# Kernel optimization log

Hardware: AMD Instinct MI355X
Metric: run time of the kernel (lower is better)

## Reference

```python
import jax, jax.numpy as jnp
import numpy as np

BN_EPS = 1e-5
LEAKY_SLOPE = 0.01

N_TOTAL, FEAT_DIM = 100000, 128
N_BATCH, K = 50000, 16
EMBED_DIM = 128


def setup_inputs() -> dict:
    key = jax.random.key(0)
    k1, k2, k3 = jax.random.split(key, 3)
    raw_features = jax.random.normal(k1, (N_TOTAL, FEAT_DIM), dtype=jnp.float32)
    weight = jax.random.normal(k2, (FEAT_DIM, EMBED_DIM), dtype=jnp.float32) * (1.0 / np.sqrt(FEAT_DIM))
    gamma = jnp.ones((EMBED_DIM,), dtype=jnp.float32)
    beta = jnp.zeros((EMBED_DIM,), dtype=jnp.float32)
    neigh_idx = jax.random.randint(k3, (N_BATCH, K), 0, N_TOTAL, dtype=jnp.int64)
    return {"raw_features": raw_features, "weight": weight, "gamma": gamma,
            "beta": beta, "neigh_idx": neigh_idx}


def reference(raw_features, weight, gamma, beta, neigh_idx):
    # Mean aggregation over sampled neighbors: [N_BATCH, K, F] -> [N_BATCH, F]
    neigh_feats = jnp.mean(raw_features[neigh_idx], axis=1)
    # Dense transform: [N_BATCH, EMBED_DIM]
    x = neigh_feats @ weight
    # BatchNorm1d (training mode: batch statistics, biased variance)
    mean = jnp.mean(x, axis=0)
    var = jnp.var(x, axis=0)
    x = (x - mean) * jax.lax.rsqrt(var + BN_EPS) * gamma + beta
    # LeakyReLU (default negative_slope=0.01)
    return jnp.where(x >= 0, x, LEAKY_SLOPE * x)
```

## Files before the change

### kernel.cpp

```cpp
#include <hip/hip_runtime.h>
#include <hip/hip_bf16.h>
#include <hip/hip_fp16.h>


#define NTOTAL 100000
#define FEAT   128
#define NB     50000
#define KNEI   16
#define NTILES (NB / 16)

#define OFF_STATS 0
#define OFF_WT    1024
#define OFF_RAWH  33792
#define OFF_NF    (33792 + 25600000)
#define WS_NEEDED (OFF_NF + 12800000)

typedef float f32x4 __attribute__((ext_vector_type(4)));
typedef short bf16x8 __attribute__((ext_vector_type(8)));
typedef _Float16 f16x8 __attribute__((ext_vector_type(8)));

__device__ __forceinline__ unsigned short f2bf(float f) {
    union { float f; unsigned u; } v; v.f = f;
    unsigned r = v.u + 0x7FFF + ((v.u >> 16) & 1);
    return (unsigned short)(r >> 16);
}

__device__ __forceinline__ unsigned h2add(unsigned a, unsigned b) {
    union { unsigned u; __half2 h; } x, y, r;
    x.u = a; y.u = b; r.h = __hadd2(x.h, y.h);
    return r.u;
}
__device__ __forceinline__ unsigned h2scale16(unsigned a) {
    union { unsigned u; __half2 h; } x, c, r;
    x.u = a; c.u = 0x2C002C00u;
    r.h = __hmul2(x.h, c.h);
    return r.u;
}

__global__ __launch_bounds__(256) void enc_conv(
    const float* __restrict__ raw, const float* __restrict__ W,
    unsigned short* __restrict__ rawh, unsigned short* __restrict__ Wt,
    float* __restrict__ gstats)
{
    const int t = threadIdx.x;
    if (blockIdx.x < 64) {
        int e = blockIdx.x * 256 + t;
        int n = e >> 7, k = e & 127;
        union { unsigned short s; __half h; } c; c.h = __float2half(W[k * FEAT + n]);
        Wt[e] = c.s;
    }
    if (blockIdx.x == 64 && t < 2 * FEAT) gstats[t] = 0.f;

    const float4* raw4 = (const float4*)raw;
    uint2* rh = (uint2*)rawh;
    const int NQ = NTOTAL * FEAT / 4;
    for (int e = blockIdx.x * 256 + t; e < NQ; e += gridDim.x * 256) {
        float4 v = raw4[e];
        union { unsigned u; __half2 h; } lo, hi;
        lo.h = __float22half2_rn(make_float2(v.x, v.y));
        hi.h = __float22half2_rn(make_float2(v.z, v.w));
        uint2 o; o.x = lo.u; o.y = hi.u;
        rh[e] = o;
    }
}

__global__ __launch_bounds__(256, 5) void enc_gather(
    const unsigned short* __restrict__ rawh, const int* __restrict__ idx,
    unsigned short* __restrict__ nf)
{
    const int t = threadIdx.x;
    const int lane = t & 63;
    const int w = (blockIdx.x * 256 + t) >> 6;
    const int r0 = w * 4;
    const int s = lane >> 4, c = lane & 15;

    const int iv = idx[r0 * KNEI + lane];

    uint4 v[16];
    #pragma unroll
    for (int k = 0; k < KNEI; ++k) {
        int ik = __shfl(iv, s * 16 + k);
        v[k] = *(const uint4*)&rawh[(size_t)ik * FEAT + c * 8];
    }
    #pragma unroll
    for (int st = 8; st >= 1; st >>= 1) {
        #pragma unroll
        for (int k = 0; k < 8; ++k) {
            if (k < st) {
                v[k].x = h2add(v[k].x, v[k + st].x);
                v[k].y = h2add(v[k].y, v[k + st].y);
                v[k].z = h2add(v[k].z, v[k + st].z);
                v[k].w = h2add(v[k].w, v[k + st].w);
            }
        }
    }
    uint4 o;
    o.x = h2scale16(v[0].x); o.y = h2scale16(v[0].y);
    o.z = h2scale16(v[0].z); o.w = h2scale16(v[0].w);
    *(uint4*)&nf[(size_t)(r0 + s) * FEAT + c * 8] = o;
}

__global__ __launch_bounds__(256, 4) void enc_mm(
    const unsigned short* __restrict__ nf, const unsigned short* __restrict__ Wt,
    float* __restrict__ out, float* __restrict__ gstats)
{
    const int t = threadIdx.x;
    const int lane = t & 63;
    const int wv = t >> 6;
    const int ln = lane & 15, qd = lane >> 4;
    const int n0 = wv * 32 + ln, n1 = n0 + 16;

    f16x8 b0[4], b1[4];
    #pragma unroll
    for (int kt = 0; kt < 4; ++kt) {
        const int k0 = kt * 32 + qd * 8;
        b0[kt] = *(const f16x8*)&Wt[n0 * FEAT + k0];
        b1[kt] = *(const f16x8*)&Wt[n1 * FEAT + k0];
    }

    float s1a = 0.f, s2a = 0.f, s1b = 0.f, s2b = 0.f;

    for (int tile = blockIdx.x; tile < NTILES; tile += gridDim.x) {
        const int i0 = tile * 16;
        f32x4 acc0 = {0.f, 0.f, 0.f, 0.f}, acc1 = {0.f, 0.f, 0.f, 0.f};
        #pragma unroll
        for (int kt = 0; kt < 4; ++kt) {
            const int k0 = kt * 32 + qd * 8;
            f16x8 a = *(const f16x8*)&nf[(size_t)(i0 + ln) * FEAT + k0];
            acc0 = __builtin_amdgcn_mfma_f32_16x16x32_f16(a, b0[kt], acc0, 0, 0, 0);
            acc1 = __builtin_amdgcn_mfma_f32_16x16x32_f16(a, b1[kt], acc1, 0, 0, 0);
        }
        #pragma unroll
        for (int ri = 0; ri < 4; ++ri) {
            const int row = i0 + qd * 4 + ri;
            float v0 = acc0[ri], v1 = acc1[ri];
            out[row * FEAT + n0] = v0;
            out[row * FEAT + n1] = v1;
            s1a += v0; s2a += v0 * v0;
            s1b += v1; s2b += v1 * v1;
        }
    }

    s1a += __shfl_down(s1a, 32); s1a += __shfl_down(s1a, 16);
    s2a += __shfl_down(s2a, 32); s2a += __shfl_down(s2a, 16);
    s1b += __shfl_down(s1b, 32); s1b += __shfl_down(s1b, 16);
    s2b += __shfl_down(s2b, 32); s2b += __shfl_down(s2b, 16);
    if (qd == 0) {
        atomicAdd(&gstats[n0], s1a);
        atomicAdd(&gstats[FEAT + n0], s2a);
        atomicAdd(&gstats[n1], s1b);
        atomicAdd(&gstats[FEAT + n1], s2b);
    }
}

__global__ __launch_bounds__(256) void enc_bn(
    float* __restrict__ out, const float* __restrict__ gstats,
    const float* __restrict__ gamma, const float* __restrict__ beta)
{
    __shared__ float sScale[FEAT], sShift[FEAT];
    const int t = threadIdx.x;
    if (t < FEAT) {
        float s1 = gstats[t], s2 = gstats[FEAT + t];
        float mean = s1 * (1.0f / NB);
        float var = s2 * (1.0f / NB) - mean * mean;
        float sc = gamma[t] * rsqrtf(var + 1e-5f);
        sScale[t] = sc;
        sShift[t] = beta[t] - mean * sc;
    }
    __syncthreads();
    const int f4 = (t & 31) * 4;
    const float4 sc = *(const float4*)&sScale[f4];
    const float4 sh = *(const float4*)&sShift[f4];
    const int total4 = NB * FEAT / 4;
    float4* o4 = (float4*)out;
    for (int e = blockIdx.x * 256 + t; e < total4; e += gridDim.x * 256) {
        float4 v = o4[e];
        float4 r; float y;
        y = v.x * sc.x + sh.x; r.x = (y >= 0.f) ? y : 0.01f * y;
        y = v.y * sc.y + sh.y; r.y = (y >= 0.f) ? y : 0.01f * y;
        y = v.z * sc.z + sh.z; r.z = (y >= 0.f) ? y : 0.01f * y;
        y = v.w * sc.w + sh.w; r.w = (y >= 0.f) ? y : 0.01f * y;
        o4[e] = r;
    }
}

#define WT_LD 136
#define A_LD  136
__global__ __launch_bounds__(256, 4) void enc_gemm_f(
    const float* __restrict__ raw, const float* __restrict__ W,
    const int* __restrict__ idx, float* __restrict__ out,
    float* __restrict__ gstats)
{
    __shared__ unsigned short sWt[128 * WT_LD];
    __shared__ unsigned short sA[16 * A_LD];
    __shared__ int sidx[256];
    const int t = threadIdx.x;
    #pragma unroll 4
    for (int i = 0; i < 64; ++i) {
        int e = t + i * 256;
        int f = e >> 7, n = e & 127;
        sWt[n * WT_LD + f] = f2bf(W[e]);
    }
    const int lane = t & 63, wv = t >> 6, ln = lane & 15, qd = lane >> 4;
    const int c = t & 31, g = t >> 5;
    const int n0 = wv * 32 + ln, n1 = n0 + 16;
    float s1a = 0.f, s2a = 0.f, s1b = 0.f, s2b = 0.f;
    const float4* raw4 = (const float4*)raw;
    for (int tile = blockIdx.x; tile < NTILES; tile += gridDim.x) {
        const int i0 = tile * 16;
        __syncthreads();
        sidx[t] = idx[i0 * KNEI + t];
        __syncthreads();
        #pragma unroll
        for (int rr = 0; rr < 2; ++rr) {
            const int r = g * 2 + rr;
            const int* ip = &sidx[r * KNEI];
            float4 acc = {0.f, 0.f, 0.f, 0.f};
            #pragma unroll
            for (int k = 0; k < KNEI; ++k) {
                float4 v = raw4[(size_t)ip[k] * 32 + c];
                acc.x += v.x; acc.y += v.y; acc.z += v.z; acc.w += v.w;
            }
            ushort4 b;
            b.x = f2bf(acc.x * 0.0625f); b.y = f2bf(acc.y * 0.0625f);
            b.z = f2bf(acc.z * 0.0625f); b.w = f2bf(acc.w * 0.0625f);
            *(ushort4*)&sA[r * A_LD + c * 4] = b;
        }
        __syncthreads();
        f32x4 acc0 = {0.f, 0.f, 0.f, 0.f}, acc1 = {0.f, 0.f, 0.f, 0.f};
        #pragma unroll
        for (int kt = 0; kt < 4; ++kt) {
            const int k0 = kt * 32 + qd * 8;
            bf16x8 a  = *(const bf16x8*)&sA[ln * A_LD + k0];
            bf16x8 bb0 = *(const bf16x8*)&sWt[n0 * WT_LD + k0];
            bf16x8 bb1 = *(const bf16x8*)&sWt[n1 * WT_LD + k0];
            acc0 = __builtin_amdgcn_mfma_f32_16x16x32_bf16(a, bb0, acc0, 0, 0, 0);
            acc1 = __builtin_amdgcn_mfma_f32_16x16x32_bf16(a, bb1, acc1, 0, 0, 0);
        }
        #pragma unroll
        for (int ri = 0; ri < 4; ++ri) {
            const int row = i0 + qd * 4 + ri;
            float v0 = acc0[ri], v1 = acc1[ri];
            out[row * FEAT + n0] = v0;
            out[row * FEAT + n1] = v1;
            s1a += v0; s2a += v0 * v0;
            s1b += v1; s2b += v1 * v1;
        }
    }
    s1a += __shfl_down(s1a, 32); s1a += __shfl_down(s1a, 16);
    s2a += __shfl_down(s2a, 32); s2a += __shfl_down(s2a, 16);
    s1b += __shfl_down(s1b, 32); s1b += __shfl_down(s1b, 16);
    s2b += __shfl_down(s2b, 32); s2b += __shfl_down(s2b, 16);
    if (qd == 0) {
        atomicAdd(&gstats[n0], s1a);
        atomicAdd(&gstats[FEAT + n0], s2a);
        atomicAdd(&gstats[n1], s1b);
        atomicAdd(&gstats[FEAT + n1], s2b);
    }
}

extern "C" void kernel_launch(void* const* d_in, const int* in_sizes, int n_in,
                              void* d_out, int out_size, void* d_ws, size_t ws_size,
                              hipStream_t stream) {
    const float* raw   = (const float*)d_in[0];
    const float* W     = (const float*)d_in[1];
    const float* gamma = (const float*)d_in[2];
    const float* beta  = (const float*)d_in[3];
    const int*   idx   = (const int*)d_in[4];
    float* out = (float*)d_out;

    char* ws = (char*)d_ws;
    float* gstats = (float*)(ws + OFF_STATS);

    if (ws_size >= WS_NEEDED) {
        unsigned short* Wt   = (unsigned short*)(ws + OFF_WT);
        unsigned short* rawh = (unsigned short*)(ws + OFF_RAWH);
        unsigned short* nf   = (unsigned short*)(ws + OFF_NF);
        enc_conv<<<2048, 256, 0, stream>>>(raw, W, rawh, Wt, gstats);
        enc_gather<<<3125, 256, 0, stream>>>(rawh, idx, nf);
        enc_mm<<<782, 256, 0, stream>>>(nf, Wt, out, gstats);
        enc_bn<<<1024, 256, 0, stream>>>(out, gstats, gamma, beta);
    } else {
        hipMemsetAsync(gstats, 0, 2 * FEAT * sizeof(float), stream);
        enc_gemm_f<<<1024, 256, 0, stream>>>(raw, W, idx, out, gstats);
        enc_bn<<<1024, 256, 0, stream>>>(out, gstats, gamma, beta);
    }
}
```

Baseline: 163.9 us.

## Fuse neighbor gather and GEMM into one kernel with per-wave tiles

Merges the gather/mean kernel and the MFMA matmul kernel into one. Each wave gathers a 16-row tile of fp16 features into shared memory and immediately multiplies it against W held in shared memory, so the intermediate neighbor-feature buffer never goes through global memory. BN statistics are first reduced in shared memory, then flushed with one atomic per column per block, which cuts global atomics. The trade-off is lower occupancy (launch bounds 3, larger LDS use) and a serial gather-then-MFMA step inside each wave that can expose gather latency.

```diff
diff --git a/kernel.cpp b/kernel.cpp
--- a/kernel.cpp
+++ b/kernel.cpp
@@ -12,19 +12,19 @@
 #define OFF_STATS 0
 #define OFF_WT    1024
 #define OFF_RAWH  33792
-#define OFF_NF    (33792 + 25600000)
-#define WS_NEEDED (OFF_NF + 12800000)
+#define WS_NEEDED (OFF_RAWH + 25600000)
 
 typedef float f32x4 __attribute__((ext_vector_type(4)));
 typedef short bf16x8 __attribute__((ext_vector_type(8)));
 typedef _Float16 f16x8 __attribute__((ext_vector_type(8)));
+
+#define ALD 136
 
 __device__ __forceinline__ unsigned short f2bf(float f) {
     union { float f; unsigned u; } v; v.f = f;
     unsigned r = v.u + 0x7FFF + ((v.u >> 16) & 1);
     return (unsigned short)(r >> 16);
 }
-
 __device__ __forceinline__ unsigned h2add(unsigned a, unsigned b) {
     union { unsigned u; __half2 h; } x, y, r;
     x.u = a; y.u = b; r.h = __hadd2(x.h, y.h);
@@ -64,93 +64,116 @@
     }
 }
 
-__global__ __launch_bounds__(256, 5) void enc_gather(
-    const unsigned short* __restrict__ rawh, const int* __restrict__ idx,
-    unsigned short* __restrict__ nf)
+__global__ __launch_bounds__(256, 3) void enc_fused(
+    const unsigned short* __restrict__ rawh, const unsigned short* __restrict__ Wt,
+    const int* __restrict__ idx, float* __restrict__ out,
+    float* __restrict__ gstats)
 {
-    const int t = threadIdx.x;
-    const int lane = t & 63;
-    const int w = (blockIdx.x * 256 + t) >> 6;
-    const int r0 = w * 4;
-    const int s = lane >> 4, c = lane & 15;
-
-    const int iv = idx[r0 * KNEI + lane];
-
-    uint4 v[16];
-    #pragma unroll
-    for (int k = 0; k < KNEI; ++k) {
-        int ik = __shfl(iv, s * 16 + k);
-        v[k] = *(const uint4*)&rawh[(size_t)ik * FEAT + c * 8];
-    }
-    #pragma unroll
-    for (int st = 8; st >= 1; st >>= 1) {
-        #pragma unroll
-        for (int k = 0; k < 8; ++k) {
-            if (k < st) {
-                v[k].x = h2add(v[k].x, v[k + st].x);
-                v[k].y = h2add(v[k].y, v[k + st].y);
-                v[k].z = h2add(v[k].z, v[k + st].z);
-                v[k].w = h2add(v[k].w, v[k + st].w);
-            }
-        }
-    }
-    uint4 o;
-    o.x = h2scale16(v[0].x); o.y = h2scale16(v[0].y);
-    o.z = h2scale16(v[0].z); o.w = h2scale16(v[0].w);
-    *(uint4*)&nf[(size_t)(r0 + s) * FEAT + c * 8] = o;
-}
-
-__global__ __launch_bounds__(256, 4) void enc_mm(
-    const unsigned short* __restrict__ nf, const unsigned short* __restrict__ Wt,
-    float* __restrict__ out, float* __restrict__ gstats)
-{
+    __shared__ unsigned short sWt[128 * ALD];
+    __shared__ unsigned short sA[4 * 16 * ALD];
+    __shared__ float sStats[2 * FEAT];
+
     const int t = threadIdx.x;
     const int lane = t & 63;
     const int wv = t >> 6;
-    const int ln = lane & 15, qd = lane >> 4;
-    const int n0 = wv * 32 + ln, n1 = n0 + 16;
-
-    f16x8 b0[4], b1[4];
+    const int ln = lane & 15;
+    const int qd = lane >> 4;
+
     #pragma unroll
-    for (int kt = 0; kt < 4; ++kt) {
-        const int k0 = kt * 32 + qd * 8;
-        b0[kt] = *(const f16x8*)&Wt[n0 * FEAT + k0];
-        b1[kt] = *(const f16x8*)&Wt[n1 * FEAT + k0];
-    }
-
-    float s1a = 0.f, s2a = 0.f, s1b = 0.f, s2b = 0.f;
-
-    for (int tile = blockIdx.x; tile < NTILES; tile += gridDim.x) {
+    for (int i = 0; i < 8; ++i) {
+        int ch = t + i * 256;
+        int n = ch >> 4, c4 = ch & 15;
+        *(uint4*)&sWt[n * ALD + c4 * 8] = *(const uint4*)&Wt[n * 128 + c4 * 8];
+    }
+    sStats[t] = 0.f;
+    __syncthreads();
+
+    unsigned short* sAw = &sA[wv * 16 * ALD];
+
+    float s1[8], s2[8];
+    #pragma unroll
+    for (int nt = 0; nt < 8; ++nt) { s1[nt] = 0.f; s2[nt] = 0.f; }
+
+    for (int tile = blockIdx.x * 4 + wv; tile < NTILES; tile += gridDim.x * 4) {
         const int i0 = tile * 16;
-        f32x4 acc0 = {0.f, 0.f, 0.f, 0.f}, acc1 = {0.f, 0.f, 0.f, 0.f};
-        #pragma unroll
-        for (int kt = 0; kt < 4; ++kt) {
-            const int k0 = kt * 32 + qd * 8;
-            f16x8 a = *(const f16x8*)&nf[(size_t)(i0 + ln) * FEAT + k0];
-            acc0 = __builtin_amdgcn_mfma_f32_16x16x32_f16(a, b0[kt], acc0, 0, 0, 0);
-            acc1 = __builtin_amdgcn_mfma_f32_16x16x32_f16(a, b1[kt], acc1, 0, 0, 0);
-        }
-        #pragma unroll
-        for (int ri = 0; ri < 4; ++ri) {
-            const int row = i0 + qd * 4 + ri;
-            float v0 = acc0[ri], v1 = acc1[ri];
-            out[row * FEAT + n0] = v0;
-            out[row * FEAT + n1] = v1;
-            s1a += v0; s2a += v0 * v0;
-            s1b += v1; s2b += v1 * v1;
-        }
-    }
-
-    s1a += __shfl_down(s1a, 32); s1a += __shfl_down(s1a, 16);
-    s2a += __shfl_down(s2a, 32); s2a += __shfl_down(s2a, 16);
-    s1b += __shfl_down(s1b, 32); s1b += __shfl_down(s1b, 16);
-    s2b += __shfl_down(s2b, 32); s2b += __shfl_down(s2b, 16);
+
+        int iva[4];
+        *(int4*)iva = ((const int4*)idx)[tile * 64 + lane];
+
+        #pragma unroll
+        for (int i = 0; i < 4; ++i) {
+            const int r = qd + i * 4;
+            uint4 v[16];
+            #pragma unroll
+            for (int k = 0; k < KNEI; ++k) {
+                int ik = __shfl(iva[k & 3], r * 4 + (k >> 2));
+                unsigned off = (unsigned)ik * FEAT + ln * 8;
+                v[k] = *(const uint4*)&rawh[off];
+            }
+            #pragma unroll
+            for (int st = 8; st >= 1; st >>= 1) {
+                #pragma unroll
+                for (int k = 0; k < 8; ++k) {
+                    if (k < st) {
+                        v[k].x = h2add(v[k].x, v[k + st].x);
+                        v[k].y = h2add(v[k].y, v[k + st].y);
+                        v[k].z = h2add(v[k].z, v[k + st].z);
+                        v[k].w = h2add(v[k].w, v[k + st].w);
+                    }
+                }
+            }
+            uint4 o;
+            o.x = h2scale16(v[0].x); o.y = h2scale16(v[0].y);
+            o.z = h2scale16(v[0].z); o.w = h2scale16(v[0].w);
+            *(uint4*)&sAw[r * ALD + ln * 8] = o;
+        }
+
+        __asm__ __volatile__("s_waitcnt lgkmcnt(0)");
+
+        f16x8 a[4];
+        #pragma unroll
+        for (int kt = 0; kt < 4; ++kt)
+            a[kt] = *(const f16x8*)&sAw[ln * ALD + kt * 32 + qd * 8];
+
+        f32x4 acc[8];
+        #pragma unroll
+        for (int nt = 0; nt < 8; ++nt) acc[nt] = (f32x4){0.f, 0.f, 0.f, 0.f};
+        #pragma unroll
+        for (int nt = 0; nt < 8; ++nt) {
+            #pragma unroll
+            for (int kt = 0; kt < 4; ++kt) {
+                f16x8 b = *(const f16x8*)&sWt[(nt * 16 + ln) * ALD + kt * 32 + qd * 8];
+                acc[nt] = __builtin_amdgcn_mfma_f32_16x16x32_f16(a[kt], b, acc[nt], 0, 0, 0);
+            }
+        }
+
+        #pragma unroll
+        for (int nt = 0; nt < 8; ++nt) {
+            const int col = nt * 16 + ln;
+            #pragma unroll
+            for (int ri = 0; ri < 4; ++ri) {
+                const int row = i0 + qd * 4 + ri;
+                float v = acc[nt][ri];
+                out[row * FEAT + col] = v;
+                s1[nt] += v; s2[nt] += v * v;
+            }
+        }
+    }
+
+    #pragma unroll
+    for (int nt = 0; nt < 8; ++nt) {
+        s1[nt] += __shfl_down(s1[nt], 32); s1[nt] += __shfl_down(s1[nt], 16);
+        s2[nt] += __shfl_down(s2[nt], 32); s2[nt] += __shfl_down(s2[nt], 16);
+    }
     if (qd == 0) {
-        atomicAdd(&gstats[n0], s1a);
-        atomicAdd(&gstats[FEAT + n0], s2a);
-        atomicAdd(&gstats[n1], s1b);
-        atomicAdd(&gstats[FEAT + n1], s2b);
-    }
+        #pragma unroll
+        for (int nt = 0; nt < 8; ++nt) {
+            atomicAdd(&sStats[nt * 16 + ln], s1[nt]);
+            atomicAdd(&sStats[FEAT + nt * 16 + ln], s2[nt]);
+        }
+    }
+    __syncthreads();
+    atomicAdd(&gstats[t], sStats[t]);
 }
 
 __global__ __launch_bounds__(256) void enc_bn(
@@ -192,7 +215,7 @@
     float* __restrict__ gstats)
 {
     __shared__ unsigned short sWt[128 * WT_LD];
-    __shared__ unsigned short sA[16 * A_LD];
+    __shared__ unsigned short sA2[16 * A_LD];
     __shared__ int sidx[256];
     const int t = threadIdx.x;
     #pragma unroll 4
@@ -224,18 +247,18 @@
             ushort4 b;
             b.x = f2bf(acc.x * 0.0625f); b.y = f2bf(acc.y * 0.0625f);
             b.z = f2bf(acc.z * 0.0625f); b.w = f2bf(acc.w * 0.0625f);
-            *(ushort4*)&sA[r * A_LD + c * 4] = b;
+            *(ushort4*)&sA2[r * A_LD + c * 4] = b;
         }
         __syncthreads();
         f32x4 acc0 = {0.f, 0.f, 0.f, 0.f}, acc1 = {0.f, 0.f, 0.f, 0.f};
         #pragma unroll
         for (int kt = 0; kt < 4; ++kt) {
             const int k0 = kt * 32 + qd * 8;
-            bf16x8 a  = *(const bf16x8*)&sA[ln * A_LD + k0];
+            bf16x8 aa  = *(const bf16x8*)&sA2[ln * A_LD + k0];
             bf16x8 bb0 = *(const bf16x8*)&sWt[n0 * WT_LD + k0];
             bf16x8 bb1 = *(const bf16x8*)&sWt[n1 * WT_LD + k0];
-            acc0 = __builtin_amdgcn_mfma_f32_16x16x32_bf16(a, bb0, acc0, 0, 0, 0);
-            acc1 = __builtin_amdgcn_mfma_f32_16x16x32_bf16(a, bb1, acc1, 0, 0, 0);
+            acc0 = __builtin_amdgcn_mfma_f32_16x16x32_bf16(aa, bb0, acc0, 0, 0, 0);
+            acc1 = __builtin_amdgcn_mfma_f32_16x16x32_bf16(aa, bb1, acc1, 0, 0, 0);
         }
         #pragma unroll
         for (int ri = 0; ri < 4; ++ri) {
@@ -275,10 +298,8 @@
     if (ws_size >= WS_NEEDED) {
         unsigned short* Wt   = (unsigned short*)(ws + OFF_WT);
         unsigned short* rawh = (unsigned short*)(ws + OFF_RAWH);
-        unsigned short* nf   = (unsigned short*)(ws + OFF_NF);
         enc_conv<<<2048, 256, 0, stream>>>(raw, W, rawh, Wt, gstats);
-        enc_gather<<<3125, 256, 0, stream>>>(rawh, idx, nf);
-        enc_mm<<<782, 256, 0, stream>>>(nf, Wt, out, gstats);
+        enc_fused<<<768, 256, 0, stream>>>(rawh, Wt, idx, out, gstats);
         enc_bn<<<1024, 256, 0, stream>>>(out, gstats, gamma, beta);
     } else {
         hipMemsetAsync(gstats, 0, 2 * FEAT * sizeof(float), stream);
```

Measured after the change: 153.5 us. -6.4%, faster.

## Partition fp16 features into column slabs with XCC-affine gather work queues

Applied to the files above, without the earlier changes.

The conversion kernel now writes the fp16 feature table as 8 column partitions of 16 features each, transposed through shared memory. The gather kernel reads its XCC id and takes tiles from per-partition atomic work queues, so each XCC's random gathers stay within one 3.2 MB slab that can fit in its L2. The matmul also writes fp16 pre-BN activations to a scratch buffer that the BN kernel reads back, which halves that intermediate traffic. In exchange the gather issues more, smaller 16-byte loads per row plus shuffle reductions, takes an atomic per queue chunk, and the intermediate activations lose precision by being stored in fp16.

```diff
diff --git a/kernel.cpp b/kernel.cpp
--- a/kernel.cpp
+++ b/kernel.cpp
@@ -10,10 +10,12 @@
 #define NTILES (NB / 16)
 
 #define OFF_STATS 0
-#define OFF_WT    1024
-#define OFF_RAWH  33792
-#define OFF_NF    (33792 + 25600000)
-#define WS_NEEDED (OFF_NF + 12800000)
+#define OFF_QCNT  1024
+#define OFF_WT    2048
+#define OFF_RAWP  34816
+#define OFF_NF    (34816 + 25600000)
+#define OFF_XH    (34816 + 25600000 + 12800000)
+#define WS_NEEDED (OFF_XH + 12800000)
 
 typedef float f32x4 __attribute__((ext_vector_type(4)));
 typedef short bf16x8 __attribute__((ext_vector_type(8)));
@@ -24,7 +26,6 @@
     unsigned r = v.u + 0x7FFF + ((v.u >> 16) & 1);
     return (unsigned short)(r >> 16);
 }
-
 __device__ __forceinline__ unsigned h2add(unsigned a, unsigned b) {
     union { unsigned u; __half2 h; } x, y, r;
     x.u = a; y.u = b; r.h = __hadd2(x.h, y.h);
@@ -36,12 +37,18 @@
     r.h = __hmul2(x.h, c.h);
     return r.u;
 }
+__device__ __forceinline__ unsigned packh2(float a, float b) {
+    union { unsigned u; __half2 h; } r;
+    r.h = __float22half2_rn(make_float2(a, b));
+    return r.u;
+}
 
 __global__ __launch_bounds__(256) void enc_conv(
     const float* __restrict__ raw, const float* __restrict__ W,
-    unsigned short* __restrict__ rawh, unsigned short* __restrict__ Wt,
-    float* __restrict__ gstats)
-{
+    unsigned short* __restrict__ rawp, unsigned short* __restrict__ Wt,
+    float* __restrict__ gstats, int* __restrict__ qcnt)
+{
+    __shared__ unsigned sT[16][68];
     const int t = threadIdx.x;
     if (blockIdx.x < 64) {
         int e = blockIdx.x * 256 + t;
@@ -50,59 +57,91 @@
         Wt[e] = c.s;
     }
     if (blockIdx.x == 64 && t < 2 * FEAT) gstats[t] = 0.f;
+    if (blockIdx.x == 65 && t < 16) qcnt[t] = 0;
 
     const float4* raw4 = (const float4*)raw;
-    uint2* rh = (uint2*)rawh;
-    const int NQ = NTOTAL * FEAT / 4;
-    for (int e = blockIdx.x * 256 + t; e < NQ; e += gridDim.x * 256) {
-        float4 v = raw4[e];
-        union { unsigned u; __half2 h; } lo, hi;
-        lo.h = __float22half2_rn(make_float2(v.x, v.y));
-        hi.h = __float22half2_rn(make_float2(v.z, v.w));
-        uint2 o; o.x = lo.u; o.y = hi.u;
-        rh[e] = o;
-    }
-}
-
-__global__ __launch_bounds__(256, 5) void enc_gather(
-    const unsigned short* __restrict__ rawh, const int* __restrict__ idx,
-    unsigned short* __restrict__ nf)
-{
-    const int t = threadIdx.x;
-    const int lane = t & 63;
-    const int w = (blockIdx.x * 256 + t) >> 6;
-    const int r0 = w * 4;
-    const int s = lane >> 4, c = lane & 15;
-
-    const int iv = idx[r0 * KNEI + lane];
-
-    uint4 v[16];
-    #pragma unroll
-    for (int k = 0; k < KNEI; ++k) {
-        int ik = __shfl(iv, s * 16 + k);
-        v[k] = *(const uint4*)&rawh[(size_t)ik * FEAT + c * 8];
-    }
-    #pragma unroll
-    for (int st = 8; st >= 1; st >>= 1) {
-        #pragma unroll
-        for (int k = 0; k < 8; ++k) {
-            if (k < st) {
-                v[k].x = h2add(v[k].x, v[k + st].x);
-                v[k].y = h2add(v[k].y, v[k + st].y);
-                v[k].z = h2add(v[k].z, v[k + st].z);
-                v[k].w = h2add(v[k].w, v[k + st].w);
+    const int pp = t >> 5, nl = (t >> 1) & 15, hh = t & 1;
+    for (int b = blockIdx.x; b < NTOTAL / 16; b += gridDim.x) {
+        const int n0 = b * 16;
+        __syncthreads();
+        #pragma unroll
+        for (int i = 0; i < 2; ++i) {
+            int e = t + i * 256;
+            int n = e >> 5, c = e & 31;
+            float4 v = raw4[(size_t)(n0 + n) * 32 + c];
+            sT[n][c * 2]     = packh2(v.x, v.y);
+            sT[n][c * 2 + 1] = packh2(v.z, v.w);
+        }
+        __syncthreads();
+        uint4 o;
+        o.x = sT[nl][pp * 8 + hh * 4 + 0];
+        o.y = sT[nl][pp * 8 + hh * 4 + 1];
+        o.z = sT[nl][pp * 8 + hh * 4 + 2];
+        o.w = sT[nl][pp * 8 + hh * 4 + 3];
+        *(uint4*)&rawp[((size_t)pp * NTOTAL + n0 + nl) * 16 + hh * 8] = o;
+    }
+}
+
+__global__ __launch_bounds__(256) void enc_gather_p(
+    const unsigned short* __restrict__ rawp, const int* __restrict__ idx,
+    unsigned short* __restrict__ nf, int* __restrict__ qcnt)
+{
+    __shared__ int sBase;
+    int xcc;
+    __asm__ __volatile__("s_getreg_b32 %0, hwreg(HW_REG_XCC_ID)" : "=s"(xcc));
+    xcc &= 7;
+
+    const int t = threadIdx.x, lane = t & 63, wv = t >> 6;
+    const int h = lane & 1, k0 = (lane >> 1) & 7, rl = lane >> 4;
+    const int comp = k0 & 3;
+
+    for (int j = 0; j < 8; ++j) {
+        const int p2 = (xcc + j) & 7;
+        const unsigned short* rp = rawp + (size_t)p2 * NTOTAL * 16;
+        while (true) {
+            __syncthreads();
+            if (t == 0) sBase = atomicAdd(&qcnt[p2], 8);
+            __syncthreads();
+            const int base = sBase;
+            if (base >= NTILES) break;
+            int lim = base + 8; if (lim > NTILES) lim = NTILES;
+            for (int tile = base; tile < lim; ++tile) {
+                int4 iva = ((const int4*)idx)[tile * 64 + wv * 16 + (lane & 15)];
+                uint4 s = {0u, 0u, 0u, 0u};
+                #pragma unroll
+                for (int kk = 0; kk < 2; ++kk) {
+                    const int k = k0 + kk * 8;
+                    const int e = rl * 16 + k;
+                    const int src = e >> 2;
+                    int c0 = __shfl(iva.x, src), c1 = __shfl(iva.y, src);
+                    int c2 = __shfl(iva.z, src), c3 = __shfl(iva.w, src);
+                    int ik = comp == 0 ? c0 : comp == 1 ? c1 : comp == 2 ? c2 : c3;
+                    uint4 v = *(const uint4*)&rp[(size_t)ik * 16 + h * 8];
+                    s.x = h2add(s.x, v.x); s.y = h2add(s.y, v.y);
+                    s.z = h2add(s.z, v.z); s.w = h2add(s.w, v.w);
+                }
+                #pragma unroll
+                for (int d = 2; d <= 8; d <<= 1) {
+                    s.x = h2add(s.x, __shfl_xor(s.x, d));
+                    s.y = h2add(s.y, __shfl_xor(s.y, d));
+                    s.z = h2add(s.z, __shfl_xor(s.z, d));
+                    s.w = h2add(s.w, __shfl_xor(s.w, d));
+                }
+                if (k0 == 0) {
+                    uint4 o;
+                    o.x = h2scale16(s.x); o.y = h2scale16(s.y);
+                    o.z = h2scale16(s.z); o.w = h2scale16(s.w);
+                    const int row = tile * 16 + wv * 4 + rl;
+                    *(uint4*)&nf[(size_t)row * FEAT + p2 * 16 + h * 8] = o;
+                }
             }
         }
     }
-    uint4 o;
-    o.x = h2scale16(v[0].x); o.y = h2scale16(v[0].y);
-    o.z = h2scale16(v[0].z); o.w = h2scale16(v[0].w);
-    *(uint4*)&nf[(size_t)(r0 + s) * FEAT + c * 8] = o;
 }
 
 __global__ __launch_bounds__(256, 4) void enc_mm(
     const unsigned short* __restrict__ nf, const unsigned short* __restrict__ Wt,
-    float* __restrict__ out, float* __restrict__ gstats)
+    unsigned short* __restrict__ xh, float* __restrict__ gstats)
 {
     const int t = threadIdx.x;
     const int lane = t & 63;
@@ -134,8 +173,10 @@
         for (int ri = 0; ri < 4; ++ri) {
             const int row = i0 + qd * 4 + ri;
             float v0 = acc0[ri], v1 = acc1[ri];
-            out[row * FEAT + n0] = v0;
-            out[row * FEAT + n1] = v1;
+            union { unsigned short s; __half h; } q0, q1;
+            q0.h = __float2half(v0); q1.h = __float2half(v1);
+            xh[row * FEAT + n0] = q0.s;
+            xh[row * FEAT + n1] = q1.s;
             s1a += v0; s2a += v0 * v0;
             s1b += v1; s2b += v1 * v1;
         }
@@ -153,7 +194,125 @@
     }
 }
 
-__global__ __launch_bounds__(256) void enc_bn(
+__global__ __launch_bounds__(256) void enc_bn_h(
+    const unsigned short* __restrict__ xh, float* __restrict__ out,
+    const float* __restrict__ gstats,
+    const float* __restrict__ gamma, const float* __restrict__ beta)
+{
+    __shared__ float sScale[FEAT], sShift[FEAT];
+    const int t = threadIdx.x;
+    if (t < FEAT) {
+        float s1 = gstats[t], s2 = gstats[FEAT + t];
+        float mean = s1 * (1.0f / NB);
+        float var = s2 * (1.0f / NB) - mean * mean;
+        float sc = gamma[t] * rsqrtf(var + 1e-5f);
+        sScale[t] = sc;
+        sShift[t] = beta[t] - mean * sc;
+    }
+    __syncthreads();
+    const int f8 = (t & 15) * 8;
+    const float4 sc0 = *(const float4*)&sScale[f8], sc1 = *(const float4*)&sScale[f8 + 4];
+    const float4 sh0 = *(const float4*)&sShift[f8], sh1 = *(const float4*)&sShift[f8 + 4];
+
+    const uint4* x4 = (const uint4*)xh;
+    float4* o4 = (float4*)out;
+    const int total8 = NB * FEAT / 8;
+    for (int e = blockIdx.x * 256 + t; e < total8; e += gridDim.x * 256) {
+        uint4 v = x4[e];
+        union { unsigned u; __half2 h; } w;
+        float4 r0, r1; float2 f; float y;
+        w.u = v.x; f = __half22float2(w.h);
+        y = f.x * sc0.x + sh0.x; r0.x = (y >= 0.f) ? y : 0.01f * y;
+        y = f.y * sc0.y + sh0.y; r0.y = (y >= 0.f) ? y : 0.01f * y;
+        w.u = v.y; f = __half22float2(w.h);
+        y = f.x * sc0.z + sh0.z; r0.z = (y >= 0.f) ? y : 0.01f * y;
+        y = f.y * sc0.w + sh0.w; r0.w = (y >= 0.f) ? y : 0.01f * y;
+        w.u = v.z; f = __half22float2(w.h);
+        y = f.x * sc1.x + sh1.x; r1.x = (y >= 0.f) ? y : 0.01f * y;
+        y = f.y * sc1.y + sh1.y; r1.y = (y >= 0.f) ? y : 0.01f * y;
+        w.u = v.w; f = __half22float2(w.h);
+        y = f.x * sc1.z + sh1.z; r1.z = (y >= 0.f) ? y : 0.01f * y;
+        y = f.y * sc1.w + sh1.w; r1.w = (y >= 0.f) ? y : 0.01f * y;
+        o4[e * 2] = r0; o4[e * 2 + 1] = r1;
+    }
+}
+
+#define WT_LD 136
+#define A_LD  136
+__global__ __launch_bounds__(256, 4) void enc_gemm_f(
+    const float* __restrict__ raw, const float* __restrict__ W,
+    const int* __restrict__ idx, float* __restrict__ out,
+    float* __restrict__ gstats)
+{
+    __shared__ unsigned short sWt[128 * WT_LD];
+    __shared__ unsigned short sA2[16 * A_LD];
+    __shared__ int sidx[256];
+    const int t = threadIdx.x;
+    #pragma unroll 4
+    for (int i = 0; i < 64; ++i) {
+        int e = t + i * 256;
+        int f = e >> 7, n = e & 127;
+        sWt[n * WT_LD + f] = f2bf(W[e]);
+    }
+    const int lane = t & 63, wv = t >> 6, ln = lane & 15, qd = lane >> 4;
+    const int c = t & 31, g = t >> 5;
+    const int n0 = wv * 32 + ln, n1 = n0 + 16;
+    float s1a = 0.f, s2a = 0.f, s1b = 0.f, s2b = 0.f;
+    const float4* raw4 = (const float4*)raw;
+    for (int tile = blockIdx.x; tile < NTILES; tile += gridDim.x) {
+        const int i0 = tile * 16;
+        __syncthreads();
+        sidx[t] = idx[i0 * KNEI + t];
+        __syncthreads();
+        #pragma unroll
+        for (int rr = 0; rr < 2; ++rr) {
+            const int r = g * 2 + rr;
+            const int* ip = &sidx[r * KNEI];
+            float4 acc = {0.f, 0.f, 0.f, 0.f};
+            #pragma unroll
+            for (int k = 0; k < KNEI; ++k) {
+                float4 v = raw4[(size_t)ip[k] * 32 + c];
+                acc.x += v.x; acc.y += v.y; acc.z += v.z; acc.w += v.w;
+            }
+            ushort4 b;
+            b.x = f2bf(acc.x * 0.0625f); b.y = f2bf(acc.y * 0.0625f);
+            b.z = f2bf(acc.z * 0.0625f); b.w = f2bf(acc.w * 0.0625f);
+            *(ushort4*)&sA2[r * A_LD + c * 4] = b;
+        }
+        __syncthreads();
+        f32x4 acc0 = {0.f, 0.f, 0.f, 0.f}, acc1 = {0.f, 0.f, 0.f, 0.f};
+        #pragma unroll
+        for (int kt = 0; kt < 4; ++kt) {
+            const int k0 = kt * 32 + qd * 8;
+            bf16x8 aa  = *(const bf16x8*)&sA2[ln * A_LD + k0];
+            bf16x8 bb0 = *(const bf16x8*)&sWt[n0 * WT_LD + k0];
+            bf16x8 bb1 = *(const bf16x8*)&sWt[n1 * WT_LD + k0];
+            acc0 = __builtin_amdgcn_mfma_f32_16x16x32_bf16(aa, bb0, acc0, 0, 0, 0);
+            acc1 = __builtin_amdgcn_mfma_f32_16x16x32_bf16(aa, bb1, acc1, 0, 0, 0);
+        }
+        #pragma unroll
+        for (int ri = 0; ri < 4; ++ri) {
+            const int row = i0 + qd * 4 + ri;
+            float v0 = acc0[ri], v1 = acc1[ri];
+            out[row * FEAT + n0] = v0;
+            out[row * FEAT + n1] = v1;
+            s1a += v0; s2a += v0 * v0;
+            s1b += v1; s2b += v1 * v1;
+        }
+    }
+    s1a += __shfl_down(s1a, 32); s1a += __shfl_down(s1a, 16);
+    s2a += __shfl_down(s2a, 32); s2a += __shfl_down(s2a, 16);
+    s1b += __shfl_down(s1b, 32); s1b += __shfl_down(s1b, 16);
+    s2b += __shfl_down(s2b, 32); s2b += __shfl_down(s2b, 16);
+    if (qd == 0) {
+        atomicAdd(&gstats[n0], s1a);
+        atomicAdd(&gstats[FEAT + n0], s2a);
+        atomicAdd(&gstats[n1], s1b);
+        atomicAdd(&gstats[FEAT + n1], s2b);
+    }
+}
+
+__global__ __launch_bounds__(256) void enc_bn_f(
     float* __restrict__ out, const float* __restrict__ gstats,
     const float* __restrict__ gamma, const float* __restrict__ beta)
 {
@@ -184,81 +343,6 @@
     }
 }
 
-#define WT_LD 136
-#define A_LD  136
-__global__ __launch_bounds__(256, 4) void enc_gemm_f(
-    const float* __restrict__ raw, const float* __restrict__ W,
-    const int* __restrict__ idx, float* __restrict__ out,
-    float* __restrict__ gstats)
-{
-    __shared__ unsigned short sWt[128 * WT_LD];
-    __shared__ unsigned short sA[16 * A_LD];
-    __shared__ int sidx[256];
-    const int t = threadIdx.x;
-    #pragma unroll 4
-    for (int i = 0; i < 64; ++i) {
-        int e = t + i * 256;
-        int f = e >> 7, n = e & 127;
-        sWt[n * WT_LD + f] = f2bf(W[e]);
-    }
-    const int lane = t & 63, wv = t >> 6, ln = lane & 15, qd = lane >> 4;
-    const int c = t & 31, g = t >> 5;
-    const int n0 = wv * 32 + ln, n1 = n0 + 16;
-    float s1a = 0.f, s2a = 0.f, s1b = 0.f, s2b = 0.f;
-    const float4* raw4 = (const float4*)raw;
-    for (int tile = blockIdx.x; tile < NTILES; tile += gridDim.x) {
-        const int i0 = tile * 16;
-        __syncthreads();
-        sidx[t] = idx[i0 * KNEI + t];
-        __syncthreads();
-        #pragma unroll
-        for (int rr = 0; rr < 2; ++rr) {
-            const int r = g * 2 + rr;
-            const int* ip = &sidx[r * KNEI];
-            float4 acc = {0.f, 0.f, 0.f, 0.f};
-            #pragma unroll
-            for (int k = 0; k < KNEI; ++k) {
-                float4 v = raw4[(size_t)ip[k] * 32 + c];
-                acc.x += v.x; acc.y += v.y; acc.z += v.z; acc.w += v.w;
-            }
-            ushort4 b;
-            b.x = f2bf(acc.x * 0.0625f); b.y = f2bf(acc.y * 0.0625f);
-            b.z = f2bf(acc.z * 0.0625f); b.w = f2bf(acc.w * 0.0625f);
-            *(ushort4*)&sA[r * A_LD + c * 4] = b;
-        }
-        __syncthreads();
-        f32x4 acc0 = {0.f, 0.f, 0.f, 0.f}, acc1 = {0.f, 0.f, 0.f, 0.f};
-        #pragma unroll
-        for (int kt = 0; kt < 4; ++kt) {
-            const int k0 = kt * 32 + qd * 8;
-            bf16x8 a  = *(const bf16x8*)&sA[ln * A_LD + k0];
-            bf16x8 bb0 = *(const bf16x8*)&sWt[n0 * WT_LD + k0];
-            bf16x8 bb1 = *(const bf16x8*)&sWt[n1 * WT_LD + k0];
-            acc0 = __builtin_amdgcn_mfma_f32_16x16x32_bf16(a, bb0, acc0, 0, 0, 0);
-            acc1 = __builtin_amdgcn_mfma_f32_16x16x32_bf16(a, bb1, acc1, 0, 0, 0);
-        }
-        #pragma unroll
-        for (int ri = 0; ri < 4; ++ri) {
-            const int row = i0 + qd * 4 + ri;
-            float v0 = acc0[ri], v1 = acc1[ri];
-            out[row * FEAT + n0] = v0;
-            out[row * FEAT + n1] = v1;
-            s1a += v0; s2a += v0 * v0;
-            s1b += v1; s2b += v1 * v1;
-        }
-    }
-    s1a += __shfl_down(s1a, 32); s1a += __shfl_down(s1a, 16);
-    s2a += __shfl_down(s2a, 32); s2a += __shfl_down(s2a, 16);
-    s1b += __shfl_down(s1b, 32); s1b += __shfl_down(s1b, 16);
-    s2b += __shfl_down(s2b, 32); s2b += __shfl_down(s2b, 16);
-    if (qd == 0) {
-        atomicAdd(&gstats[n0], s1a);
-        atomicAdd(&gstats[FEAT + n0], s2a);
-        atomicAdd(&gstats[n1], s1b);
-        atomicAdd(&gstats[FEAT + n1], s2b);
-    }
-}
-
 extern "C" void kernel_launch(void* const* d_in, const int* in_sizes, int n_in,
                               void* d_out, int out_size, void* d_ws, size_t ws_size,
                               hipStream_t stream) {
@@ -273,16 +357,18 @@
     float* gstats = (float*)(ws + OFF_STATS);
 
     if (ws_size >= WS_NEEDED) {
+        int* qcnt            = (int*)(ws + OFF_QCNT);
         unsigned short* Wt   = (unsigned short*)(ws + OFF_WT);
-        unsigned short* rawh = (unsigned short*)(ws + OFF_RAWH);
+        unsigned short* rawp = (unsigned short*)(ws + OFF_RAWP);
         unsigned short* nf   = (unsigned short*)(ws + OFF_NF);
-        enc_conv<<<2048, 256, 0, stream>>>(raw, W, rawh, Wt, gstats);
-        enc_gather<<<3125, 256, 0, stream>>>(rawh, idx, nf);
-        enc_mm<<<782, 256, 0, stream>>>(nf, Wt, out, gstats);
-        enc_bn<<<1024, 256, 0, stream>>>(out, gstats, gamma, beta);
+        unsigned short* xh   = (unsigned short*)(ws + OFF_XH);
+        enc_conv<<<2048, 256, 0, stream>>>(raw, W, rawp, Wt, gstats, qcnt);
+        enc_gather_p<<<2048, 256, 0, stream>>>(rawp, idx, nf, qcnt);
+        enc_mm<<<782, 256, 0, stream>>>(nf, Wt, xh, gstats);
+        enc_bn_h<<<1024, 256, 0, stream>>>(xh, out, gstats, gamma, beta);
     } else {
         hipMemsetAsync(gstats, 0, 2 * FEAT * sizeof(float), stream);
         enc_gemm_f<<<1024, 256, 0, stream>>>(raw, W, idx, out, gstats);
-        enc_bn<<<1024, 256, 0, stream>>>(out, gstats, gamma, beta);
-    }
-}
+        enc_bn_f<<<1024, 256, 0, stream>>>(out, gstats, gamma, beta);
+    }
+}
```

Result: slower. 374.2 us (+128.3%).
